# Performance work log

Hardware: AMD Instinct MI355X
Metric: run time of the kernel (lower is better)

The kernel has to match this reference:

```python
import jax, jax.numpy as jnp
import numpy as np

N_ATOMS = 4096
K = 24                 # exact neighbors per atom (regular neighbor list)
RC = 6.0

# sf_spec parameters (see init_kwargs)
G2_RS = jnp.array([0.5, 2.0, 3.5, 5.0], jnp.float32)
G2_ETA = jnp.array([4.0, 4.0, 4.0, 4.0], jnp.float32)
G4_LAMBD = jnp.array([1.0, 1.0, -1.0, -1.0], jnp.float32)
G4_ZETA = jnp.array([1.0, 4.0, 1.0, 4.0], jnp.float32)
G4_ETA = jnp.array([0.01, 0.05, 0.01, 0.05], jnp.float32)


def setup_inputs() -> dict:
    key = jax.random.key(0)
    k1, k2, k3, k4 = jax.random.split(key, 4)
    n_pairs = N_ATOMS * K
    i_ind = jnp.repeat(jnp.arange(N_ATOMS, dtype=jnp.int32), K)
    off = jax.random.randint(k1, (n_pairs,), 1, N_ATOMS, dtype=jnp.int32)
    j_ind = (i_ind + off) % N_ATOMS
    ind_2 = jnp.stack([i_ind, j_ind], axis=1)          # [n_pairs,2], sorted by i
    dirs = jax.random.normal(k2, (n_pairs, 3), jnp.float32)
    dirs = dirs / jnp.linalg.norm(dirs, axis=1, keepdims=True)
    r = jax.random.uniform(k3, (n_pairs,), jnp.float32, 0.8, RC - 0.1)
    diff = dirs * r[:, None]                           # [n_pairs,3], |diff| < rc
    elems = jax.random.randint(k4, (N_ATOMS,), 1, 4, dtype=jnp.int32)
    return {"ind_2": ind_2, "elems": elems, "diff": diff}


def fc_f1(dist):
    # CutoffFunc 'f1': 0.5*(cos(pi*r/rc)+1)
    return 0.5 * (jnp.cos(jnp.pi * dist / RC) + 1.0)


def form_triplet(ind_2, n_atoms):
    """Faithful _form_triplet; triplet count is static because every atom has
    exactly K = n_pairs//n_atoms neighbors."""
    n_pairs = ind_2.shape[0]
    Kn = n_pairs // n_atoms
    p_iind = ind_2[:, 0]
    p_aind = jnp.arange(1, n_pairs + 1, dtype=jnp.int32)         # cumsum(ones)
    seg_min = jax.ops.segment_min(p_aind, p_iind, num_segments=n_atoms)
    p_rind = p_aind - seg_min[p_iind]                            # rank within group
    t_dense = jnp.zeros((n_atoms, Kn), jnp.int32).at[p_iind, p_rind].set(p_aind)
    t_dense = t_dense[p_iind]                                    # [n_pairs, K]
    t_ijind = jnp.repeat(jnp.arange(n_pairs, dtype=jnp.int32), Kn)
    t_ikind = t_dense.reshape(-1) - 1                            # row-major like tf.where
    keep = jnp.nonzero(t_ijind != t_ikind, size=n_pairs * (Kn - 1))[0]
    return jnp.stack([t_ijind[keep], t_ikind[keep]], axis=1)


def g2_fp(dist, fc, i_ind, n_atoms):
    # G2_SF with i=j='ALL'
    sf = jnp.exp(-G2_ETA * (dist[:, None] - G2_RS) ** 2) * fc[:, None]
    return jax.ops.segment_sum(sf, i_ind, num_segments=n_atoms)


def g4_fp(dist, fc, diff, ind_2, ind_3, n_atoms):
    # G4_SF with i=j=k='ALL' (Behler G5-style, no jk cutoff)
    ij, ik = ind_3[:, 0], ind_3[:, 1]
    i_rind = ind_2[:, 0][ij]
    d_ij, d_ik = diff[ij], diff[ik]
    R_ij, R_ik = dist[ij], dist[ik]
    fc_ij, fc_ik = fc[ij], fc[ik]
    cos = jnp.sum(d_ij * d_ik, axis=1) / (R_ij * R_ik)
    sf = (2.0 ** (1.0 - G4_ZETA)
          * (1.0 + G4_LAMBD * cos[:, None]) ** G4_ZETA
          * jnp.exp(-G4_ETA * (R_ij ** 2 + R_ik ** 2)[:, None])
          * (fc_ij * fc_ik)[:, None])
    return jax.ops.segment_sum(sf, i_rind, num_segments=n_atoms)


def reference(ind_2, elems, diff):
    n_atoms = elems.shape[0]
    n_pairs = ind_2.shape[0]
    ind_3 = form_triplet(ind_2, n_atoms)
    i_ind = ind_2[:, 0]

    def fps_fn(d):
        # connect_dist_grad: dist recomputed from diff so grads flow
        dist = jnp.linalg.norm(d, axis=1)
        fc = fc_f1(dist)
        fp0 = g2_fp(dist, fc, i_ind, n_atoms)
        fp1 = g4_fp(dist, fc, d, ind_2, ind_3, n_atoms)
        return fp0, fp1

    fp0, fp1 = fps_fn(diff)
    # Per-column Jacobian wrt diff (each pair row feeds exactly one atom, so
    # grad of column-sum equals the per-row Jacobian entries)
    jac0, jac1 = jax.jacrev(lambda d: tuple(f.sum(0) for f in fps_fn(d)))(diff)
    jacob0 = jnp.transpose(jac0, (1, 2, 0))   # [n_pairs, 3, n_g2]
    jacob1 = jnp.transpose(jac1, (1, 2, 0))   # [n_pairs, 3, n_g4]
    p_ind = jnp.arange(n_pairs, dtype=jnp.int32)
    jacob_ind = jnp.stack([p_ind, i_ind], axis=1)  # [pair, center-atom]
    return fp0, jacob0, jacob_ind, fp1, jacob1, jacob_ind
```

## Files before the change

kernel.cpp:

```cpp
#include <hip/hip_runtime.h>

#define NA   4096
#define KN   24
#define NP   (NA*KN)
#define APB  8
#define PPB  (APB*KN)
#define NS   4
#define TPB  (NS*PPB)

#define OFF_J0   (NA*4)
#define OFF_JI   (OFF_J0 + NP*12)
#define OFF_FP1  (OFF_JI + NP*2)
#define OFF_J1   (OFF_FP1 + NA*4)
#define OFF_JI2  (OFF_J1 + NP*12)

__global__ __launch_bounds__(TPB) void bpsf_kernel(const float* __restrict__ diff,
                                                   float* __restrict__ out)
{
    const int t = threadIdx.x;
    const int s = t / PPB;
    const int u = t - s * PPB;
    const int aloc = u / KN;
    const int r = u - aloc * KN;
    const int atom = blockIdx.x * APB + aloc;
    const int p = atom * KN + r;

    __shared__ float4 s_pd[PPB];
    __shared__ float4 s_pe[PPB];
    __shared__ float  s_sf0[PPB][5];
    __shared__ float  s_sf1[PPB][5];
    __shared__ float  s_part[3*PPB][17];

    if (s == 0) {
        const float dx = diff[3*p+0];
        const float dy = diff[3*p+1];
        const float dz = diff[3*p+2];
        const float Rsq  = dx*dx + dy*dy + dz*dz;
        const float R    = sqrtf(Rsq);
        const float invR = __builtin_amdgcn_rcpf(R);
        float sn, cs;
        __sincosf(0.52359877559829887f * R, &sn, &cs);
        const float fc  = 0.5f * (cs + 1.0f);
        const float fcp = -0.26179938779914943f * sn;

        s_pd[u] = make_float4(dx, dy, dz, R);
        s_pe[u] = make_float4(invR, fc, fcp, Rsq);

        const float rs[4] = {0.5f, 2.0f, 3.5f, 5.0f};
        float j0[12];
        #pragma unroll
        for (int m = 0; m < 4; ++m) {
            const float dr = R - rs[m];
            const float g  = __expf(-4.0f * dr * dr);
            s_sf0[u][m] = g * fc;
            const float coef = invR * g * (fcp - 8.0f * dr * fc);
            j0[0*4+m] = dx * coef;
            j0[1*4+m] = dy * coef;
            j0[2*4+m] = dz * coef;
        }
        float4* o = (float4*)(out + OFF_J0 + p * 12);
        o[0] = make_float4(j0[0], j0[1], j0[2],  j0[3]);
        o[1] = make_float4(j0[4], j0[5], j0[6],  j0[7]);
        o[2] = make_float4(j0[8], j0[9], j0[10], j0[11]);
        const float2 ji = make_float2((float)p, (float)atom);
        *(float2*)(out + OFF_JI  + 2*p) = ji;
        *(float2*)(out + OFF_JI2 + 2*p) = ji;
    }

    __syncthreads();

    const float4 pd0 = s_pd[u];
    const float4 pe0 = s_pe[u];
    const float dx = pd0.x, dy = pd0.y, dz = pd0.z;
    const float invR = pe0.x, fc = pe0.y, fcp = pe0.z, Rsq = pe0.w;
    const float invRsq = invR * invR;

    float acc[12];
    #pragma unroll
    for (int k = 0; k < 12; ++k) acc[k] = 0.0f;
    float fp1a[4] = {0.0f, 0.0f, 0.0f, 0.0f};

    const int qbase = aloc * KN;

    #pragma unroll
    for (int k = 0; k < KN/NS; ++k) {
        const int qr = NS*k + s;
        const int q  = qbase + qr;
        const float4 pd = s_pd[q];
        const float4 pe = s_pe[q];
        const float fcq = (qr == r) ? 0.0f : pe.y;
        const float qx = pd.x, qy = pd.y, qz = pd.z;
        const float Rq = pd.w, iRq = pe.x;

        const float dot   = dx*qx + dy*qy + dz*qz;
        const float iR1R2 = invR * iRq;
        const float cth   = dot * iR1R2;
        const float r2s   = Rsq + Rq * Rq;
        const float e1    = __expf(-0.01f * r2s);
        const float e1sq  = e1 * e1;
        const float e2    = e1sq * e1sq * e1;
        const float F     = fc * fcq;
        const float gterm = fcq * fcp * invR;
        const float ci    = cth * invRsq;

        {
            const float A  = 1.0f + cth;
            const float EF = e1 * F;
            const float sf = A * EF;
            fp1a[0] += sf;
            const float cq = EF * iR1R2;
            const float cp = -EF * ci - 0.02f * sf + A * e1 * gterm;
            acc[0] += cq*qx + cp*dx;
            acc[4] += cq*qy + cp*dy;
            acc[8] += cq*qz + cp*dz;
        }
        {
            const float b  = 1.0f + cth;
            const float b2 = b * b;
            const float A  = 0.125f * b2 * b2;
            const float dA = 0.5f * b2 * b;
            const float EF = e2 * F;
            const float sf = A * EF;
            fp1a[1] += sf;
            const float cq = EF * dA * iR1R2;
            const float cp = -EF * dA * ci - 0.1f * sf + A * e2 * gterm;
            acc[1] += cq*qx + cp*dx;
            acc[5] += cq*qy + cp*dy;
            acc[9] += cq*qz + cp*dz;
        }
        {
            const float A  = 1.0f - cth;
            const float EF = e1 * F;
            const float sf = A * EF;
            fp1a[2] += sf;
            const float cq = -EF * iR1R2;
            const float cp = EF * ci - 0.02f * sf + A * e1 * gterm;
            acc[2]  += cq*qx + cp*dx;
            acc[6]  += cq*qy + cp*dy;
            acc[10] += cq*qz + cp*dz;
        }
        {
            const float b  = 1.0f - cth;
            const float b2 = b * b;
            const float A  = 0.125f * b2 * b2;
            const float dA = -0.5f * b2 * b;
            const float EF = e2 * F;
            const float sf = A * EF;
            fp1a[3] += sf;
            const float cq = EF * dA * iR1R2;
            const float cp = -EF * dA * ci - 0.1f * sf + A * e2 * gterm;
            acc[3]  += cq*qx + cp*dx;
            acc[7]  += cq*qy + cp*dy;
            acc[11] += cq*qz + cp*dz;
        }
    }

    if (s) {
        float* w = s_part[(s-1)*PPB + u];
        #pragma unroll
        for (int k = 0; k < 12; ++k) w[k] = acc[k];
        #pragma unroll
        for (int m = 0; m < 4; ++m) w[12+m] = fp1a[m];
    }
    __syncthreads();

    if (s == 0) {
        #pragma unroll
        for (int g = 0; g < 3; ++g) {
            const float* w = s_part[g*PPB + u];
            #pragma unroll
            for (int k = 0; k < 12; ++k) acc[k] += w[k];
            #pragma unroll
            for (int m = 0; m < 4; ++m) fp1a[m] += w[12+m];
        }

        float4* o = (float4*)(out + OFF_J1 + p * 12);
        o[0] = make_float4(2.0f*acc[0], 2.0f*acc[1], 2.0f*acc[2],  2.0f*acc[3]);
        o[1] = make_float4(2.0f*acc[4], 2.0f*acc[5], 2.0f*acc[6],  2.0f*acc[7]);
        o[2] = make_float4(2.0f*acc[8], 2.0f*acc[9], 2.0f*acc[10], 2.0f*acc[11]);

        s_sf1[u][0] = fp1a[0]; s_sf1[u][1] = fp1a[1];
        s_sf1[u][2] = fp1a[2]; s_sf1[u][3] = fp1a[3];
    }
    __syncthreads();

    if (t < APB * 4) {
        const int a2 = t >> 2;
        const int m  = t & 3;
        const int src = a2 * KN;
        float s0 = 0.0f, s1 = 0.0f;
        for (int rr = 0; rr < KN; ++rr) {
            s0 += s_sf0[src + rr][m];
            s1 += s_sf1[src + rr][m];
        }
        const int ga = blockIdx.x * APB + a2;
        out[ga * 4 + m]           = s0;
        out[OFF_FP1 + ga * 4 + m] = s1;
    }
}

extern "C" void kernel_launch(void* const* d_in, const int* in_sizes, int n_in,
                              void* d_out, int out_size, void* d_ws, size_t ws_size,
                              hipStream_t stream) {
    const float* diff = (const float*)d_in[2];
    float* out = (float*)d_out;
    bpsf_kernel<<<NA / APB, TPB, 0, stream>>>(diff, out);
}
```

Before: 14.86 us.

## Factor G4 triplet Jacobian into per-pair sums with per-pair precomputed exponentials

Uses the separability exp(-eta(Rij^2+Rik^2)) = exp(-eta Rij^2) * exp(-eta Rik^2) to precompute per-pair weights (fc*E1, fc*E2, fcp*E) and unit vectors in shared memory, which removes the per-triplet exponential. The inner loop now accumulates a small set of sums (vector sums, cos-weighted scalars, fingerprints), and the per-pair Jacobian is assembled once after the cross-slice reduction. This cuts per-triplet arithmetic and transcendental work. In exchange the partial-sum buffer grows from 16 to 20 floats per thread and register pressure rises, and the reassociated float maths may change rounding slightly.

```diff
diff --git a/kernel.cpp b/kernel.cpp
--- a/kernel.cpp
+++ b/kernel.cpp
@@ -13,6 +13,7 @@
 #define OFF_FP1  (OFF_JI + NP*2)
 #define OFF_J1   (OFF_FP1 + NA*4)
 #define OFF_JI2  (OFF_J1 + NP*12)
+
 
 __global__ __launch_bounds__(TPB) void bpsf_kernel(const float* __restrict__ diff,
                                                    float* __restrict__ out)
@@ -26,25 +27,34 @@
     const int p = atom * KN + r;
 
     __shared__ float4 s_pd[PPB];
-    __shared__ float4 s_pe[PPB];
+    __shared__ float  s_w2[PPB];
+    __shared__ float2 s_g[PPB];
+    __shared__ float2 s_ri[PPB];
     __shared__ float  s_sf0[PPB][5];
     __shared__ float  s_sf1[PPB][5];
-    __shared__ float  s_part[3*PPB][17];
+    __shared__ float  s_part[3*PPB][21];
+
+    float R=0.f, invR=0.f;
 
     if (s == 0) {
         const float dx = diff[3*p+0];
         const float dy = diff[3*p+1];
         const float dz = diff[3*p+2];
-        const float Rsq  = dx*dx + dy*dy + dz*dz;
-        const float R    = sqrtf(Rsq);
-        const float invR = __builtin_amdgcn_rcpf(R);
+        const float Rsq = dx*dx + dy*dy + dz*dz;
+        R    = sqrtf(Rsq);
+        invR = __builtin_amdgcn_rcpf(R);
         float sn, cs;
         __sincosf(0.52359877559829887f * R, &sn, &cs);
         const float fc  = 0.5f * (cs + 1.0f);
         const float fcp = -0.26179938779914943f * sn;
-
-        s_pd[u] = make_float4(dx, dy, dz, R);
-        s_pe[u] = make_float4(invR, fc, fcp, Rsq);
+        const float E1  = __expf(-0.01f * Rsq);
+        const float e1s = E1 * E1;
+        const float E2  = e1s * e1s * E1;
+
+        s_pd[u] = make_float4(dx*invR, dy*invR, dz*invR, fc*E1);
+        s_w2[u] = fc * E2;
+        s_g[u]  = make_float2(fcp*E1, fcp*E2);
+        s_ri[u] = make_float2(R, invR);
 
         const float rs[4] = {0.5f, 2.0f, 3.5f, 5.0f};
         float j0[12];
@@ -69,16 +79,16 @@
 
     __syncthreads();
 
-    const float4 pd0 = s_pd[u];
-    const float4 pe0 = s_pe[u];
-    const float dx = pd0.x, dy = pd0.y, dz = pd0.z;
-    const float invR = pe0.x, fc = pe0.y, fcp = pe0.z, Rsq = pe0.w;
-    const float invRsq = invR * invR;
-
-    float acc[12];
-    #pragma unroll
-    for (int k = 0; k < 12; ++k) acc[k] = 0.0f;
-    float fp1a[4] = {0.0f, 0.0f, 0.0f, 0.0f};
+    const float4 pr = s_pd[u];
+    const float ux = pr.x, uy = pr.y, uz = pr.z;
+    const float W1p = pr.w;
+    const float W2p = s_w2[u];
+    const float2 gg = s_g[u];
+    const float G1p = gg.x, G2p = gg.y;
+
+    float V1x=0,V1y=0,V1z=0, V2x=0,V2y=0,V2z=0, V3x=0,V3y=0,V3z=0;
+    float S1=0,S2=0,S3=0, QH1=0,QcH1=0,Q1=0,Q3=0;
+    float F0=0,F1=0,F2=0,F3=0;
 
     const int qbase = aloc * KN;
 
@@ -86,81 +96,51 @@
     for (int k = 0; k < KN/NS; ++k) {
         const int qr = NS*k + s;
         const int q  = qbase + qr;
-        const float4 pd = s_pd[q];
-        const float4 pe = s_pe[q];
-        const float fcq = (qr == r) ? 0.0f : pe.y;
-        const float qx = pd.x, qy = pd.y, qz = pd.z;
-        const float Rq = pd.w, iRq = pe.x;
-
-        const float dot   = dx*qx + dy*qy + dz*qz;
-        const float iR1R2 = invR * iRq;
-        const float cth   = dot * iR1R2;
-        const float r2s   = Rsq + Rq * Rq;
-        const float e1    = __expf(-0.01f * r2s);
-        const float e1sq  = e1 * e1;
-        const float e2    = e1sq * e1sq * e1;
-        const float F     = fc * fcq;
-        const float gterm = fcq * fcp * invR;
-        const float ci    = cth * invRsq;
-
-        {
-            const float A  = 1.0f + cth;
-            const float EF = e1 * F;
-            const float sf = A * EF;
-            fp1a[0] += sf;
-            const float cq = EF * iR1R2;
-            const float cp = -EF * ci - 0.02f * sf + A * e1 * gterm;
-            acc[0] += cq*qx + cp*dx;
-            acc[4] += cq*qy + cp*dy;
-            acc[8] += cq*qz + cp*dz;
-        }
-        {
-            const float b  = 1.0f + cth;
-            const float b2 = b * b;
-            const float A  = 0.125f * b2 * b2;
-            const float dA = 0.5f * b2 * b;
-            const float EF = e2 * F;
-            const float sf = A * EF;
-            fp1a[1] += sf;
-            const float cq = EF * dA * iR1R2;
-            const float cp = -EF * dA * ci - 0.1f * sf + A * e2 * gterm;
-            acc[1] += cq*qx + cp*dx;
-            acc[5] += cq*qy + cp*dy;
-            acc[9] += cq*qz + cp*dz;
-        }
-        {
-            const float A  = 1.0f - cth;
-            const float EF = e1 * F;
-            const float sf = A * EF;
-            fp1a[2] += sf;
-            const float cq = -EF * iR1R2;
-            const float cp = EF * ci - 0.02f * sf + A * e1 * gterm;
-            acc[2]  += cq*qx + cp*dx;
-            acc[6]  += cq*qy + cp*dy;
-            acc[10] += cq*qz + cp*dz;
-        }
-        {
-            const float b  = 1.0f - cth;
-            const float b2 = b * b;
-            const float A  = 0.125f * b2 * b2;
-            const float dA = -0.5f * b2 * b;
-            const float EF = e2 * F;
-            const float sf = A * EF;
-            fp1a[3] += sf;
-            const float cq = EF * dA * iR1R2;
-            const float cp = -EF * dA * ci - 0.1f * sf + A * e2 * gterm;
-            acc[3]  += cq*qx + cp*dx;
-            acc[7]  += cq*qy + cp*dy;
-            acc[11] += cq*qz + cp*dz;
-        }
+        const float4 qd = s_pd[q];
+        const bool self = (qr == r);
+        const float W1q = self ? 0.0f : qd.w;
+        const float W2q = self ? 0.0f : s_w2[q];
+        const float qx = qd.x, qy = qd.y, qz = qd.z;
+
+        const float c   = ux*qx + uy*qy + uz*qz;
+        const float P1  = W1p * W1q;
+        const float P2  = W2p * W2q;
+        const float H1  = G1p * W1q;
+        const float H2  = G2p * W2q;
+
+        const float cP1 = c * P1;
+        F0 += P1 + cP1;
+        F2 += P1 - cP1;
+        S1 += cP1;
+        QH1  += H1;
+        QcH1 += c * H1;
+        V1x += P1*qx; V1y += P1*qy; V1z += P1*qz;
+
+        const float bp  = 1.0f + c, bm = 1.0f - c;
+        const float bp2 = bp*bp,    bm2 = bm*bm;
+        const float bp4 = bp2*bp2,  bm4 = bm2*bm2;
+        const float A1  = 0.125f * bp4;
+        const float A3  = 0.125f * bm4;
+        const float d1h = bp2 * bp;
+        const float d3h = bm2 * bm;
+        const float a1  = P2 * d1h;
+        const float a3  = P2 * d3h;
+        F1 += A1 * P2;
+        F3 += A3 * P2;
+        S2 += a1 * c;
+        S3 += a3 * c;
+        Q1 += A1 * H2;
+        Q3 += A3 * H2;
+        V2x += a1*qx; V2y += a1*qy; V2z += a1*qz;
+        V3x += a3*qx; V3y += a3*qy; V3z += a3*qz;
     }
 
     if (s) {
         float* w = s_part[(s-1)*PPB + u];
-        #pragma unroll
-        for (int k = 0; k < 12; ++k) w[k] = acc[k];
-        #pragma unroll
-        for (int m = 0; m < 4; ++m) w[12+m] = fp1a[m];
+        w[0]=V1x; w[1]=V1y; w[2]=V1z; w[3]=V2x; w[4]=V2y; w[5]=V2z;
+        w[6]=V3x; w[7]=V3y; w[8]=V3z; w[9]=S1; w[10]=S2; w[11]=S3;
+        w[12]=QH1; w[13]=QcH1; w[14]=Q1; w[15]=Q3;
+        w[16]=F0; w[17]=F1; w[18]=F2; w[19]=F3;
     }
     __syncthreads();
 
@@ -168,19 +148,38 @@
         #pragma unroll
         for (int g = 0; g < 3; ++g) {
             const float* w = s_part[g*PPB + u];
-            #pragma unroll
-            for (int k = 0; k < 12; ++k) acc[k] += w[k];
-            #pragma unroll
-            for (int m = 0; m < 4; ++m) fp1a[m] += w[12+m];
+            V1x+=w[0]; V1y+=w[1]; V1z+=w[2]; V2x+=w[3]; V2y+=w[4]; V2z+=w[5];
+            V3x+=w[6]; V3y+=w[7]; V3z+=w[8]; S1+=w[9]; S2+=w[10]; S3+=w[11];
+            QH1+=w[12]; QcH1+=w[13]; Q1+=w[14]; Q3+=w[15];
+            F0+=w[16]; F1+=w[17]; F2+=w[18]; F3+=w[19];
         }
 
+        const float iR  = invR;
+        const float iRh = 0.5f * invR;
+        const float t0 = -0.02f * R * F0 + (QH1 + QcH1);
+        const float t2 = -0.02f * R * F2 + (QH1 - QcH1);
+        const float t1 = -0.10f * R * F1 + Q1;
+        const float t3 = -0.10f * R * F3 + Q3;
+
+        const float a0x = iR *(V1x - S1*ux) + t0*ux;
+        const float a0y = iR *(V1y - S1*uy) + t0*uy;
+        const float a0z = iR *(V1z - S1*uz) + t0*uz;
+        const float a1x = iRh*(V2x - S2*ux) + t1*ux;
+        const float a1y = iRh*(V2y - S2*uy) + t1*uy;
+        const float a1z = iRh*(V2z - S2*uz) + t1*uz;
+        const float a2x = -iR *(V1x - S1*ux) + t2*ux;
+        const float a2y = -iR *(V1y - S1*uy) + t2*uy;
+        const float a2z = -iR *(V1z - S1*uz) + t2*uz;
+        const float a3x = -iRh*(V3x - S3*ux) + t3*ux;
+        const float a3y = -iRh*(V3y - S3*uy) + t3*uy;
+        const float a3z = -iRh*(V3z - S3*uz) + t3*uz;
+
         float4* o = (float4*)(out + OFF_J1 + p * 12);
-        o[0] = make_float4(2.0f*acc[0], 2.0f*acc[1], 2.0f*acc[2],  2.0f*acc[3]);
-        o[1] = make_float4(2.0f*acc[4], 2.0f*acc[5], 2.0f*acc[6],  2.0f*acc[7]);
-        o[2] = make_float4(2.0f*acc[8], 2.0f*acc[9], 2.0f*acc[10], 2.0f*acc[11]);
-
-        s_sf1[u][0] = fp1a[0]; s_sf1[u][1] = fp1a[1];
-        s_sf1[u][2] = fp1a[2]; s_sf1[u][3] = fp1a[3];
+        o[0] = make_float4(2.0f*a0x, 2.0f*a1x, 2.0f*a2x, 2.0f*a3x);
+        o[1] = make_float4(2.0f*a0y, 2.0f*a1y, 2.0f*a2y, 2.0f*a3y);
+        o[2] = make_float4(2.0f*a0z, 2.0f*a1z, 2.0f*a2z, 2.0f*a3z);
+
+        s_sf1[u][0]=F0; s_sf1[u][1]=F1; s_sf1[u][2]=F2; s_sf1[u][3]=F3;
     }
     __syncthreads();
 
```

After: 13.59 us. -8.6%, faster.
